# Optimization experiments

Hardware: AMD Instinct MI355X
Metric: run time of the kernel (lower is better)

The kernel has to match this reference:

```python
import jax, jax.numpy as jnp
import numpy as np

N_SRC = 50000
N_DST = 50000
N_EDGES = 1600000
D_IN = 128
K = 8          # num_heads
D_OUT = 16     # out_dim per head (K*D_OUT = 128)
NEG_SLOPE = 0.2


def setup_inputs() -> dict:
    key = jax.random.key(0)
    ks = jax.random.split(key, 8)
    feat_src = jax.random.normal(ks[0], (N_SRC, D_IN), dtype=jnp.float32)
    feat_dst = jax.random.normal(ks[1], (N_DST, D_IN), dtype=jnp.float32)
    W_src = jax.random.normal(ks[2], (D_IN, K * D_OUT), dtype=jnp.float32) * (1.0 / np.sqrt(D_IN))
    b_src = jnp.zeros((K * D_OUT,), dtype=jnp.float32)
    W_dst = jax.random.normal(ks[3], (D_IN, K * D_OUT), dtype=jnp.float32) * (1.0 / np.sqrt(D_IN))
    b_dst = jnp.zeros((K * D_OUT,), dtype=jnp.float32)
    attn_src = jax.random.normal(ks[4], (K, 2 * D_OUT), dtype=jnp.float32) * 0.1
    src_idx = jax.random.randint(ks[5], (N_EDGES,), 0, N_SRC, dtype=jnp.int64)
    dst_idx = jax.random.randint(ks[6], (N_EDGES,), 0, N_DST, dtype=jnp.int64)
    return {"feat_src": feat_src, "feat_dst": feat_dst, "W_src": W_src, "b_src": b_src,
            "W_dst": W_dst, "b_dst": b_dst, "attn_src": attn_src,
            "src_idx": src_idx, "dst_idx": dst_idx}


def reference(feat_src, feat_dst, W_src, b_src, W_dst, b_dst, attn_src, src_idx, dst_idx):
    n_dst = feat_dst.shape[0]
    # feat_drop is identity (p=0). Linear projections, reshape to heads.
    hs = (feat_src @ W_src + b_src).reshape(-1, K, D_OUT)  # [N_src, K, D_out]
    hd = (feat_dst @ W_dst + b_dst).reshape(-1, K, D_OUT)  # [N_dst, K, D_out]
    # per-node attention logits
    el = jnp.sum(hs * attn_src[:, :D_OUT], axis=-1)  # [N_src, K]
    er = jnp.sum(hd * attn_src[:, D_OUT:], axis=-1)  # [N_dst, K]
    # per-edge score: u_add_v then LeakyReLU
    e = el[src_idx] + er[dst_idx]                    # [E, K]
    e = jnp.where(e >= 0, e, NEG_SLOPE * e)
    # edge softmax over incoming edges of each dst node (numerically stable)
    emax = jax.ops.segment_max(e, dst_idx, num_segments=n_dst)
    emax = jnp.where(jnp.isfinite(emax), emax, 0.0)  # handle dsts with no edges
    ee = jnp.exp(e - emax[dst_idx])                  # [E, K]
    esum = jax.ops.segment_sum(ee, dst_idx, num_segments=n_dst)
    a = ee / esum[dst_idx]                           # [E, K]
    # weighted message aggregation: u_mul_e then sum over incoming edges
    m = hs[src_idx] * a[:, :, None]                  # [E, K, D_out]
    out = jax.ops.segment_sum(m, dst_idx, num_segments=n_dst)  # [N_dst, K, D_out]
    return out.reshape(n_dst, K * D_OUT)
```

## Files before the change

kernel.cpp:

```cpp
#include <hip/hip_runtime.h>
#include <hip/hip_bf16.h>
#include <hip/hip_fp16.h>

#define NEG_SLOPE 0.2f
#define EPB   8192
#define CAP   4096
#define MAXC  1024

typedef __attribute__((ext_vector_type(8))) short bf16x8;
typedef __attribute__((ext_vector_type(4))) float f32x4;

__device__ __forceinline__ float b2f_lo(unsigned u) { return __uint_as_float(u << 16); }
__device__ __forceinline__ float b2f_hi(unsigned u) { return __uint_as_float(u & 0xffff0000u); }

__device__ __forceinline__ short f2b(float x) {
    unsigned u = __float_as_uint(x);
    unsigned r = (u + 0x7fffu + ((u >> 16) & 1u)) >> 16;
    return (short)r;
}

__global__ __launch_bounds__(256) void pack_kernel(
    const float* __restrict__ W_src, const float* __restrict__ W_dst,
    const float* __restrict__ b_src, const float* __restrict__ b_dst,
    const float* __restrict__ attn,
    uint4* __restrict__ wp_src, uint4* __restrict__ wp_dst,
    float* __restrict__ c_all,
    int* __restrict__ cursor, int nCoarse)
{
    const int e = blockIdx.x * 256 + threadIdx.x;
    if (e < 4608) {
        const int which = e / 2304;
        const int e2 = e % 2304;
        const float* W = which ? W_dst : W_src;
        uint4* wp = which ? wp_dst : wp_src;
        const int aoff = which ? 16 : 0;
        short out[8];
        if (e2 < 2048) {
            const int t = e2 >> 8, q = (e2 >> 6) & 3, l = e2 & 63;
            const int kbase = (l >> 4) * 8 + q * 32;
            const int n = t * 16 + (l & 15);
            #pragma unroll
            for (int j = 0; j < 8; ++j) out[j] = f2b(W[(size_t)(kbase + j) * 128 + n]);
            *(uint4*)&wp[(t * 4 + q) * 64 + l] = *(uint4*)out;
        } else {
            const int e3 = e2 - 2048;
            const int q = e3 >> 6, l = e3 & 63;
            const int kbase = (l >> 4) * 8 + q * 32;
            const int n = l & 15;
            #pragma unroll
            for (int j = 0; j < 8; ++j) {
                float v = 0.f;
                if (n < 8) {
                    for (int dd = 0; dd < 16; ++dd)
                        v += W[(size_t)(kbase + j) * 128 + n * 16 + dd] * attn[n * 32 + aoff + dd];
                }
                out[j] = f2b(v);
            }
            *(uint4*)&wp[(32 + q) * 64 + l] = *(uint4*)out;
        }
    } else if (e < 4624) {
        const int k = e - 4608;
        const int which = k >> 3, kk = k & 7;
        const float* bb = which ? b_dst : b_src;
        const int aoff = which ? 16 : 0;
        float v = 0.f;
        for (int dd = 0; dd < 16; ++dd) v += bb[kk * 16 + dd] * attn[kk * 32 + aoff + dd];
        c_all[k] = v;
    } else if (e < 4624 + nCoarse) {
        const int c = e - 4624;
        cursor[c] = c * CAP;
    }
}

__device__ __forceinline__ void scatter_body(
    const int* __restrict__ src_idx, const int* __restrict__ dst_idx,
    int* __restrict__ cursor, int* __restrict__ coarse,
    int nEdges, int nCoarse, int bx)
{
    __shared__ int lcnt[MAXC];
    __shared__ int lbase[MAXC];
    const int t = threadIdx.x;
    for (int i = t; i < nCoarse; i += 256) lcnt[i] = 0;
    __syncthreads();
    const int e0 = bx * EPB;
    const int e1 = min(e0 + EPB, nEdges);
    for (int e = e0 + t; e < e1; e += 256) atomicAdd(&lcnt[dst_idx[e] >> 6], 1);
    __syncthreads();
    for (int i = t; i < nCoarse; i += 256) {
        const int c = lcnt[i];
        lbase[i] = c ? atomicAdd(&cursor[i], c) : 0;
        lcnt[i] = 0;
    }
    __syncthreads();
    for (int e = e0 + t; e < e1; e += 256) {
        const int d = dst_idx[e];
        const int s = src_idx[e];
        const int bin = d >> 6;
        const int lr = atomicAdd(&lcnt[bin], 1);
        const int pos = lbase[bin] + lr;
        if (pos < (bin + 1) * CAP)
            coarse[pos] = (s << 6) | (d & 63);
    }
}

template<bool STORE_H>
__device__ __forceinline__ void proj_body(
    const float* __restrict__ feat, const uint4* __restrict__ wp,
    const float* __restrict__ b, const float* __restrict__ cvec,
    short* __restrict__ hs_out, float* __restrict__ el_out,
    int N, int bx)
{
    const int t = threadIdx.x;
    const int lane = t & 63;
    const int w = t >> 6;
    const int m  = lane & 15;
    const int q8 = lane >> 4;
    const int row0 = bx * 128 + w * 32;

    f32x4 acc0[9], acc1[9];
    #pragma unroll
    for (int tt = 0; tt < 8; ++tt) {
        const float bn = b[tt * 16 + m];
        acc0[tt] = (f32x4){bn, bn, bn, bn};
        acc1[tt] = (f32x4){bn, bn, bn, bn};
    }
    acc0[8] = (f32x4){0.f, 0.f, 0.f, 0.f};
    acc1[8] = (f32x4){0.f, 0.f, 0.f, 0.f};

    int rowA0 = row0 + m;      if (rowA0 >= N) rowA0 = N - 1;
    int rowA1 = row0 + 16 + m; if (rowA1 >= N) rowA1 = N - 1;
    const float* f0 = feat + (size_t)rowA0 * 128 + q8 * 8;
    const float* f1 = feat + (size_t)rowA1 * 128 + q8 * 8;
    const bf16x8* wpv = (const bf16x8*)wp;

    #pragma unroll
    for (int kc = 0; kc < 4; ++kc) {
        const float4 fa0 = *(const float4*)(f0 + kc * 32);
        const float4 fb0 = *(const float4*)(f0 + kc * 32 + 4);
        const float4 fa1 = *(const float4*)(f1 + kc * 32);
        const float4 fb1 = *(const float4*)(f1 + kc * 32 + 4);
        bf16x8 a0, a1;
        a0[0]=f2b(fa0.x); a0[1]=f2b(fa0.y); a0[2]=f2b(fa0.z); a0[3]=f2b(fa0.w);
        a0[4]=f2b(fb0.x); a0[5]=f2b(fb0.y); a0[6]=f2b(fb0.z); a0[7]=f2b(fb0.w);
        a1[0]=f2b(fa1.x); a1[1]=f2b(fa1.y); a1[2]=f2b(fa1.z); a1[3]=f2b(fa1.w);
        a1[4]=f2b(fb1.x); a1[5]=f2b(fb1.y); a1[6]=f2b(fb1.z); a1[7]=f2b(fb1.w);
        #pragma unroll
        for (int tt = 0; tt < 8; ++tt) {
            const bf16x8 bf = wpv[(tt * 4 + kc) * 64 + lane];
            acc0[tt] = __builtin_amdgcn_mfma_f32_16x16x32_bf16(a0, bf, acc0[tt], 0, 0, 0);
            acc1[tt] = __builtin_amdgcn_mfma_f32_16x16x32_bf16(a1, bf, acc1[tt], 0, 0, 0);
        }
        {
            const bf16x8 bv = wpv[(32 + kc) * 64 + lane];
            acc0[8] = __builtin_amdgcn_mfma_f32_16x16x32_bf16(a0, bv, acc0[8], 0, 0, 0);
            acc1[8] = __builtin_amdgcn_mfma_f32_16x16x32_bf16(a1, bv, acc1[8], 0, 0, 0);
        }
    }

    #pragma unroll
    for (int half = 0; half < 2; ++half) {
        const f32x4* acc = half ? acc1 : acc0;
        const int rbase = row0 + half * 16 + q8 * 4;
        #pragma unroll
        for (int reg = 0; reg < 4; ++reg) {
            const int row = rbase + reg;
            if (row < N) {
                if (STORE_H) {
                    #pragma unroll
                    for (int tt = 0; tt < 8; ++tt)
                        hs_out[(size_t)row * 128 + tt * 16 + m] = f2b(acc[tt][reg]);
                }
                if (m < 8) el_out[(size_t)row * 8 + m] = acc[8][reg] + cvec[m];
            }
        }
    }
}

__global__ __launch_bounds__(256, 2) void fused_kernel(
    const float* __restrict__ feat_src, const float* __restrict__ feat_dst,
    const uint4* __restrict__ wp_src, const uint4* __restrict__ wp_dst,
    const float* __restrict__ b_src, const float* __restrict__ b_dst,
    const float* __restrict__ c_all,
    short* __restrict__ hs, float* __restrict__ el, float* __restrict__ er,
    const int* __restrict__ src_idx, const int* __restrict__ dst_idx,
    int* __restrict__ cursor, int* __restrict__ coarse,
    int n_src, int n_dst, int nEdges, int nCoarse, int nSB, int pSrcBlocks)
{
    int bx = blockIdx.x;
    if (bx < nSB) { scatter_body(src_idx, dst_idx, cursor, coarse, nEdges, nCoarse, bx); return; }
    bx -= nSB;
    if (bx < pSrcBlocks) {
        proj_body<true>(feat_src, wp_src, b_src, c_all, hs, el, n_src, bx);
        return;
    }
    bx -= pSrcBlocks;
    proj_body<false>(feat_dst, wp_dst, b_dst, c_all + 8, nullptr, er, n_dst, bx);
}

__global__ __launch_bounds__(1024) void binscan_kernel(
    const int* __restrict__ cursor, int* __restrict__ outbase,
    int* __restrict__ off, int nCoarse, int n_dst)
{
    __shared__ int buf[1024];
    const int t = threadIdx.x;
    int v = 0;
    if (t < nCoarse) {
        v = cursor[t] - t * CAP;
        v = max(0, min(v, CAP));
    }
    buf[t] = v;
    __syncthreads();
    #pragma unroll
    for (int s = 1; s < 1024; s <<= 1) {
        const int add = (t >= s) ? buf[t - s] : 0;
        __syncthreads();
        buf[t] += add;
        __syncthreads();
    }
    if (t < nCoarse) outbase[t] = buf[t] - v;
    if (t == nCoarse - 1) {
        outbase[nCoarse] = buf[t];
        off[n_dst] = buf[t];
    }
}

__global__ __launch_bounds__(256) void fine_sort_kernel(
    const int* __restrict__ coarse, const int* __restrict__ outbase,
    const float* __restrict__ el,
    const float* __restrict__ er,
    int* __restrict__ off, unsigned short* __restrict__ sorted_src,
    unsigned short* __restrict__ pw,
    int n_dst, int nCoarse)
{
    __shared__ int fpk[CAP];
    __shared__ int h[64];
    __shared__ int cu[64];
    __shared__ float erL[64 * 8];
    const int t = threadIdx.x, c = blockIdx.x;
    const int base_in = c * CAP;
    const int obase = outbase[c];
    const int cnt = outbase[c + 1] - obase;
    for (int i = t; i < 512; i += 256) {
        const int d = c * 64 + (i >> 3);
        erL[i] = (d < n_dst) ? er[(size_t)d * 8 + (i & 7)] : 0.f;
    }
    if (t < 64) h[t] = 0;
    __syncthreads();
    for (int i = t; i < cnt; i += 256) atomicAdd(&h[coarse[base_in + i] & 63], 1);
    __syncthreads();
    if (t == 0) {
        int run = 0;
        #pragma unroll
        for (int j = 0; j < 64; ++j) {
            cu[j] = run;
            const int d = c * 64 + j;
            if (d < n_dst) off[d] = obase + run;
            run += h[j];
        }
    }
    __syncthreads();
    for (int i = t; i < cnt; i += 256) {
        const int v = coarse[base_in + i];
        const int p = atomicAdd(&cu[v & 63], 1);
        fpk[p] = v;
    }
    __syncthreads();
    for (int i = t; i < cnt; i += 256) {
        const int v = fpk[i];
        const int s = v >> 6;
        const int dl = v & 63;
        const float4 e0 = *(const float4*)(el + (size_t)s * 8);
        const float4 e1 = *(const float4*)(el + (size_t)s * 8 + 4);
        const float xs[8] = {e0.x, e0.y, e0.z, e0.w, e1.x, e1.y, e1.z, e1.w};
        unsigned short w[8];
        #pragma unroll
        for (int k = 0; k < 8; ++k) {
            float x = xs[k] + erL[dl * 8 + k];
            x = (x >= 0.f) ? x : NEG_SLOPE * x;
            w[k] = __half_as_ushort(__float2half(__expf(x)));
        }
        *(uint4*)(pw + (size_t)(obase + i) * 8) = *(uint4*)w;
        sorted_src[obase + i] = (unsigned short)s;
    }
}

__global__ __launch_bounds__(256) void reduce_kernel(
    const unsigned short* __restrict__ sorted_src, const int* __restrict__ off,
    const unsigned short* __restrict__ hs,
    const unsigned short* __restrict__ pw,
    float* __restrict__ out,
    int n_dst)
{
    const int wid = blockIdx.x * 4 + (threadIdx.x >> 6);
    if (wid >= n_dst) return;
    const int lane = threadIdx.x & 63;
    const int sub  = lane >> 5;
    const int l32  = lane & 31;
    const int k    = l32 >> 2;
    const int k2   = k & 6;
    const int khi  = k & 1;
    const int beg = off[wid], end = off[wid + 1];

    float a0 = 0.f, a1 = 0.f, a2 = 0.f, a3 = 0.f, es = 0.f;
    int i = beg + sub;
    for (; i + 2 < end; i += 4) {
        const int sA = sorted_src[i];
        const int sB = sorted_src[i + 2];
        const unsigned wpA = *(const unsigned*)(pw + (size_t)i * 8 + k2);
        const unsigned wpB = *(const unsigned*)(pw + (size_t)(i + 2) * 8 + k2);
        const uint2 uA = ((const uint2*)(hs + (size_t)sA * 128))[l32];
        const uint2 uB = ((const uint2*)(hs + (size_t)sB * 128))[l32];
        const unsigned short usA = khi ? (unsigned short)(wpA >> 16) : (unsigned short)(wpA & 0xffff);
        const unsigned short usB = khi ? (unsigned short)(wpB >> 16) : (unsigned short)(wpB & 0xffff);
        const float eA = __half2float(__ushort_as_half(usA));
        const float eB = __half2float(__ushort_as_half(usB));
        es += eA + eB;
        a0 = fmaf(eA, b2f_lo(uA.x), a0); a1 = fmaf(eA, b2f_hi(uA.x), a1);
        a2 = fmaf(eA, b2f_lo(uA.y), a2); a3 = fmaf(eA, b2f_hi(uA.y), a3);
        a0 = fmaf(eB, b2f_lo(uB.x), a0); a1 = fmaf(eB, b2f_hi(uB.x), a1);
        a2 = fmaf(eB, b2f_lo(uB.y), a2); a3 = fmaf(eB, b2f_hi(uB.y), a3);
    }
    for (; i < end; i += 2) {
        const int s = sorted_src[i];
        const unsigned wp4 = *(const unsigned*)(pw + (size_t)i * 8 + k2);
        const uint2 u = ((const uint2*)(hs + (size_t)s * 128))[l32];
        const unsigned short us = khi ? (unsigned short)(wp4 >> 16) : (unsigned short)(wp4 & 0xffff);
        const float ee = __half2float(__ushort_as_half(us));
        es += ee;
        a0 = fmaf(ee, b2f_lo(u.x), a0); a1 = fmaf(ee, b2f_hi(u.x), a1);
        a2 = fmaf(ee, b2f_lo(u.y), a2); a3 = fmaf(ee, b2f_hi(u.y), a3);
    }
    es += __shfl_xor(es, 32);
    a0 += __shfl_xor(a0, 32);
    a1 += __shfl_xor(a1, 32);
    a2 += __shfl_xor(a2, 32);
    a3 += __shfl_xor(a3, 32);
    if (sub == 0) {
        const float inv = (es > 0.f) ? 1.f / es : 0.f;
        float4 o;
        o.x = a0 * inv; o.y = a1 * inv; o.z = a2 * inv; o.w = a3 * inv;
        *(float4*)(out + (size_t)wid * 128 + l32 * 4) = o;
    }
}

extern "C" void kernel_launch(void* const* d_in, const int* in_sizes, int n_in,
                              void* d_out, int out_size, void* d_ws, size_t ws_size,
                              hipStream_t stream) {
    const float* feat_src = (const float*)d_in[0];
    const float* feat_dst = (const float*)d_in[1];
    const float* W_src    = (const float*)d_in[2];
    const float* b_src    = (const float*)d_in[3];
    const float* W_dst    = (const float*)d_in[4];
    const float* b_dst    = (const float*)d_in[5];
    const float* attn     = (const float*)d_in[6];
    const int*   src_idx  = (const int*)d_in[7];
    const int*   dst_idx  = (const int*)d_in[8];
    float* out = (float*)d_out;

    const int n_src  = in_sizes[0] / 128;
    const int n_dst  = in_sizes[1] / 128;
    const int nEdges = in_sizes[7];

    const int nCoarse = (n_dst + 63) >> 6;
    const int nSB     = (nEdges + EPB - 1) / EPB;
    const int pSrc    = (n_src + 127) / 128;
    const int pDst    = (n_dst + 127) / 128;

    unsigned short* hs = (unsigned short*)d_ws;
    unsigned short* pw = hs + (size_t)n_src * 128;
    float* el = (float*)(pw + (size_t)nEdges * 8);
    float* er = el + (size_t)n_src * 8;
    int* off     = (int*)(er + (size_t)n_dst * 8);
    int* outbase = off + n_dst + 4;
    int* cursor  = outbase + nCoarse + 4;
    uintptr_t p = (uintptr_t)(cursor + nCoarse);
    p = (p + 15) & ~(uintptr_t)15;
    int* coarse = (int*)p;
    unsigned short* sorted_src = (unsigned short*)(coarse + (size_t)nCoarse * CAP);
    uintptr_t p2 = (uintptr_t)(sorted_src + nEdges);
    p2 = (p2 + 15) & ~(uintptr_t)15;
    uint4* wp_src = (uint4*)p2;
    uint4* wp_dst = wp_src + 36 * 64;
    float* c_all  = (float*)(wp_dst + 36 * 64);

    pack_kernel<<<22, 256, 0, stream>>>(W_src, W_dst, b_src, b_dst, attn,
                                        wp_src, wp_dst, c_all, cursor, nCoarse);

    fused_kernel<<<nSB + pSrc + pDst, 256, 0, stream>>>(
        feat_src, feat_dst, wp_src, wp_dst, b_src, b_dst, c_all,
        (short*)hs, el, er, src_idx, dst_idx, cursor, coarse,
        n_src, n_dst, nEdges, nCoarse, nSB, pSrc);

    binscan_kernel<<<1, 1024, 0, stream>>>(cursor, outbase, off, nCoarse, n_dst);

    fine_sort_kernel<<<nCoarse, 256, 0, stream>>>(coarse, outbase, el, er,
                                                  off, sorted_src, pw,
                                                  n_dst, nCoarse);

    reduce_kernel<<<(n_dst + 3) / 4, 256, 0, stream>>>(sorted_src, off,
        hs, pw, out, n_dst);
}
```

Measured before the change: 241.4 us.

## Fuse binscan, fine sort and reduce into one per-bin sort-reduce kernel

After: 238.3 us. Within noise of the previous version (-1.3%).

```diff
diff --git a/kernel.cpp b/kernel.cpp
--- a/kernel.cpp
+++ b/kernel.cpp
@@ -1,6 +1,5 @@
 #include <hip/hip_runtime.h>
 #include <hip/hip_bf16.h>
-#include <hip/hip_fp16.h>
 
 #define NEG_SLOPE 0.2f
 #define EPB   8192
@@ -197,49 +196,23 @@
     proj_body<false>(feat_dst, wp_dst, b_dst, c_all + 8, nullptr, er, n_dst, bx);
 }
 
-__global__ __launch_bounds__(1024) void binscan_kernel(
-    const int* __restrict__ cursor, int* __restrict__ outbase,
-    int* __restrict__ off, int nCoarse, int n_dst)
-{
-    __shared__ int buf[1024];
-    const int t = threadIdx.x;
-    int v = 0;
-    if (t < nCoarse) {
-        v = cursor[t] - t * CAP;
-        v = max(0, min(v, CAP));
-    }
-    buf[t] = v;
-    __syncthreads();
-    #pragma unroll
-    for (int s = 1; s < 1024; s <<= 1) {
-        const int add = (t >= s) ? buf[t - s] : 0;
-        __syncthreads();
-        buf[t] += add;
-        __syncthreads();
-    }
-    if (t < nCoarse) outbase[t] = buf[t] - v;
-    if (t == nCoarse - 1) {
-        outbase[nCoarse] = buf[t];
-        off[n_dst] = buf[t];
-    }
-}
-
-__global__ __launch_bounds__(256) void fine_sort_kernel(
-    const int* __restrict__ coarse, const int* __restrict__ outbase,
+__global__ __launch_bounds__(256) void sort_reduce_kernel(
+    const int* __restrict__ coarse, const int* __restrict__ cursor,
     const float* __restrict__ el,
     const float* __restrict__ er,
-    int* __restrict__ off, unsigned short* __restrict__ sorted_src,
-    unsigned short* __restrict__ pw,
+    const unsigned short* __restrict__ hs,
+    float* __restrict__ out,
     int n_dst, int nCoarse)
 {
     __shared__ int fpk[CAP];
     __shared__ int h[64];
+    __shared__ int lbeg[64];
     __shared__ int cu[64];
     __shared__ float erL[64 * 8];
     const int t = threadIdx.x, c = blockIdx.x;
     const int base_in = c * CAP;
-    const int obase = outbase[c];
-    const int cnt = outbase[c + 1] - obase;
+    const int cnt = min(cursor[c] - base_in, CAP);
+
     for (int i = t; i < 512; i += 256) {
         const int d = c * 64 + (i >> 3);
         erL[i] = (d < n_dst) ? er[(size_t)d * 8 + (i & 7)] : 0.f;
@@ -251,12 +224,7 @@
     if (t == 0) {
         int run = 0;
         #pragma unroll
-        for (int j = 0; j < 64; ++j) {
-            cu[j] = run;
-            const int d = c * 64 + j;
-            if (d < n_dst) off[d] = obase + run;
-            run += h[j];
-        }
+        for (int j = 0; j < 64; ++j) { cu[j] = run; lbeg[j] = run; run += h[j]; }
     }
     __syncthreads();
     for (int i = t; i < cnt; i += 256) {
@@ -265,81 +233,57 @@
         fpk[p] = v;
     }
     __syncthreads();
-    for (int i = t; i < cnt; i += 256) {
-        const int v = fpk[i];
-        const int s = v >> 6;
-        const int dl = v & 63;
-        const float4 e0 = *(const float4*)(el + (size_t)s * 8);
-        const float4 e1 = *(const float4*)(el + (size_t)s * 8 + 4);
-        const float xs[8] = {e0.x, e0.y, e0.z, e0.w, e1.x, e1.y, e1.z, e1.w};
-        unsigned short w[8];
-        #pragma unroll
-        for (int k = 0; k < 8; ++k) {
-            float x = xs[k] + erL[dl * 8 + k];
-            x = (x >= 0.f) ? x : NEG_SLOPE * x;
-            w[k] = __half_as_ushort(__float2half(__expf(x)));
-        }
-        *(uint4*)(pw + (size_t)(obase + i) * 8) = *(uint4*)w;
-        sorted_src[obase + i] = (unsigned short)s;
-    }
-}
-
-__global__ __launch_bounds__(256) void reduce_kernel(
-    const unsigned short* __restrict__ sorted_src, const int* __restrict__ off,
-    const unsigned short* __restrict__ hs,
-    const unsigned short* __restrict__ pw,
-    float* __restrict__ out,
-    int n_dst)
-{
-    const int wid = blockIdx.x * 4 + (threadIdx.x >> 6);
-    if (wid >= n_dst) return;
-    const int lane = threadIdx.x & 63;
-    const int sub  = lane >> 5;
-    const int l32  = lane & 31;
-    const int k    = l32 >> 2;
-    const int k2   = k & 6;
-    const int khi  = k & 1;
-    const int beg = off[wid], end = off[wid + 1];
-
-    float a0 = 0.f, a1 = 0.f, a2 = 0.f, a3 = 0.f, es = 0.f;
-    int i = beg + sub;
-    for (; i + 2 < end; i += 4) {
-        const int sA = sorted_src[i];
-        const int sB = sorted_src[i + 2];
-        const unsigned wpA = *(const unsigned*)(pw + (size_t)i * 8 + k2);
-        const unsigned wpB = *(const unsigned*)(pw + (size_t)(i + 2) * 8 + k2);
-        const uint2 uA = ((const uint2*)(hs + (size_t)sA * 128))[l32];
-        const uint2 uB = ((const uint2*)(hs + (size_t)sB * 128))[l32];
-        const unsigned short usA = khi ? (unsigned short)(wpA >> 16) : (unsigned short)(wpA & 0xffff);
-        const unsigned short usB = khi ? (unsigned short)(wpB >> 16) : (unsigned short)(wpB & 0xffff);
-        const float eA = __half2float(__ushort_as_half(usA));
-        const float eB = __half2float(__ushort_as_half(usB));
-        es += eA + eB;
-        a0 = fmaf(eA, b2f_lo(uA.x), a0); a1 = fmaf(eA, b2f_hi(uA.x), a1);
-        a2 = fmaf(eA, b2f_lo(uA.y), a2); a3 = fmaf(eA, b2f_hi(uA.y), a3);
-        a0 = fmaf(eB, b2f_lo(uB.x), a0); a1 = fmaf(eB, b2f_hi(uB.x), a1);
-        a2 = fmaf(eB, b2f_lo(uB.y), a2); a3 = fmaf(eB, b2f_hi(uB.y), a3);
-    }
-    for (; i < end; i += 2) {
-        const int s = sorted_src[i];
-        const unsigned wp4 = *(const unsigned*)(pw + (size_t)i * 8 + k2);
-        const uint2 u = ((const uint2*)(hs + (size_t)s * 128))[l32];
-        const unsigned short us = khi ? (unsigned short)(wp4 >> 16) : (unsigned short)(wp4 & 0xffff);
-        const float ee = __half2float(__ushort_as_half(us));
-        es += ee;
-        a0 = fmaf(ee, b2f_lo(u.x), a0); a1 = fmaf(ee, b2f_hi(u.x), a1);
-        a2 = fmaf(ee, b2f_lo(u.y), a2); a3 = fmaf(ee, b2f_hi(u.y), a3);
-    }
-    es += __shfl_xor(es, 32);
-    a0 += __shfl_xor(a0, 32);
-    a1 += __shfl_xor(a1, 32);
-    a2 += __shfl_xor(a2, 32);
-    a3 += __shfl_xor(a3, 32);
-    if (sub == 0) {
-        const float inv = (es > 0.f) ? 1.f / es : 0.f;
-        float4 o;
-        o.x = a0 * inv; o.y = a1 * inv; o.z = a2 * inv; o.w = a3 * inv;
-        *(float4*)(out + (size_t)wid * 128 + l32 * 4) = o;
+
+    const int w = t >> 6, lane = t & 63;
+    const int sub = lane >> 5;
+    const int l32 = lane & 31;
+    const int k   = l32 >> 2;
+    for (int j = 0; j < 16; ++j) {
+        const int dl = w * 16 + j;
+        const int d  = c * 64 + dl;
+        if (d >= n_dst) break;
+        const float erk = erL[dl * 8 + k];
+        const int beg = lbeg[dl], end = lbeg[dl] + h[dl];
+        float a0 = 0.f, a1 = 0.f, a2 = 0.f, a3 = 0.f, es = 0.f;
+        int i = beg + sub;
+        for (; i + 2 < end; i += 4) {
+            const int sA = fpk[i] >> 6;
+            const int sB = fpk[i + 2] >> 6;
+            const float lA = el[(size_t)sA * 8 + k];
+            const float lB = el[(size_t)sB * 8 + k];
+            const uint2 uA = ((const uint2*)(hs + (size_t)sA * 128))[l32];
+            const uint2 uB = ((const uint2*)(hs + (size_t)sB * 128))[l32];
+            float xA = lA + erk; xA = (xA >= 0.f) ? xA : NEG_SLOPE * xA;
+            float xB = lB + erk; xB = (xB >= 0.f) ? xB : NEG_SLOPE * xB;
+            const float eA = __expf(xA);
+            const float eB = __expf(xB);
+            es += eA + eB;
+            a0 = fmaf(eA, b2f_lo(uA.x), a0); a1 = fmaf(eA, b2f_hi(uA.x), a1);
+            a2 = fmaf(eA, b2f_lo(uA.y), a2); a3 = fmaf(eA, b2f_hi(uA.y), a3);
+            a0 = fmaf(eB, b2f_lo(uB.x), a0); a1 = fmaf(eB, b2f_hi(uB.x), a1);
+            a2 = fmaf(eB, b2f_lo(uB.y), a2); a3 = fmaf(eB, b2f_hi(uB.y), a3);
+        }
+        for (; i < end; i += 2) {
+            const int s = fpk[i] >> 6;
+            const float l = el[(size_t)s * 8 + k];
+            const uint2 u = ((const uint2*)(hs + (size_t)s * 128))[l32];
+            float x = l + erk; x = (x >= 0.f) ? x : NEG_SLOPE * x;
+            const float ee = __expf(x);
+            es += ee;
+            a0 = fmaf(ee, b2f_lo(u.x), a0); a1 = fmaf(ee, b2f_hi(u.x), a1);
+            a2 = fmaf(ee, b2f_lo(u.y), a2); a3 = fmaf(ee, b2f_hi(u.y), a3);
+        }
+        es += __shfl_xor(es, 32);
+        a0 += __shfl_xor(a0, 32);
+        a1 += __shfl_xor(a1, 32);
+        a2 += __shfl_xor(a2, 32);
+        a3 += __shfl_xor(a3, 32);
+        if (sub == 0) {
+            const float inv = (es > 0.f) ? 1.f / es : 0.f;
+            float4 o;
+            o.x = a0 * inv; o.y = a1 * inv; o.z = a2 * inv; o.w = a3 * inv;
+            *(float4*)(out + (size_t)d * 128 + l32 * 4) = o;
+        }
     }
 }
 
@@ -367,17 +311,13 @@
     const int pDst    = (n_dst + 127) / 128;
 
     unsigned short* hs = (unsigned short*)d_ws;
-    unsigned short* pw = hs + (size_t)n_src * 128;
-    float* el = (float*)(pw + (size_t)nEdges * 8);
+    float* el = (float*)(hs + (size_t)n_src * 128);
     float* er = el + (size_t)n_src * 8;
-    int* off     = (int*)(er + (size_t)n_dst * 8);
-    int* outbase = off + n_dst + 4;
-    int* cursor  = outbase + nCoarse + 4;
+    int* cursor = (int*)(er + (size_t)n_dst * 8);
     uintptr_t p = (uintptr_t)(cursor + nCoarse);
     p = (p + 15) & ~(uintptr_t)15;
     int* coarse = (int*)p;
-    unsigned short* sorted_src = (unsigned short*)(coarse + (size_t)nCoarse * CAP);
-    uintptr_t p2 = (uintptr_t)(sorted_src + nEdges);
+    uintptr_t p2 = (uintptr_t)(coarse + (size_t)nCoarse * CAP);
     p2 = (p2 + 15) & ~(uintptr_t)15;
     uint4* wp_src = (uint4*)p2;
     uint4* wp_dst = wp_src + 36 * 64;
@@ -391,12 +331,6 @@
         (short*)hs, el, er, src_idx, dst_idx, cursor, coarse,
         n_src, n_dst, nEdges, nCoarse, nSB, pSrc);
 
-    binscan_kernel<<<1, 1024, 0, stream>>>(cursor, outbase, off, nCoarse, n_dst);
-
-    fine_sort_kernel<<<nCoarse, 256, 0, stream>>>(coarse, outbase, el, er,
-                                                  off, sorted_src, pw,
-                                                  n_dst, nCoarse);
-
-    reduce_kernel<<<(n_dst + 3) / 4, 256, 0, stream>>>(sorted_src, off,
-        hs, pw, out, n_dst);
-}
+    sort_reduce_kernel<<<nCoarse, 256, 0, stream>>>(coarse, cursor, el, er,
+                                                    hs, out, n_dst, nCoarse);
+}
```
